# Performance work log

Measured on AMD Instinct MI355X. Metric: run time of the kernel, lower is better.

The kernel has to match this reference:

```python
import jax, jax.numpy as jnp
import numpy as np

B, K, LQ, LR, H = 32, 8, 128, 256, 512  # H = hidden_dim*2
L = LQ + K * LR


def setup_inputs() -> dict:
    key = jax.random.key(0)
    ks = jax.random.split(key, 10)
    w = 0.02
    return {
        "h_q": jax.random.normal(ks[0], (B, LQ, H), jnp.float32),
        "q_mask": jnp.ones((B, LQ), jnp.float32),
        "h_r": jax.random.normal(ks[1], (B, K, LR, H), jnp.float32),
        "r_mask": jnp.ones((B, K, LR), jnp.float32),
        "s_t": jax.random.normal(ks[2], (B, H), jnp.float32),
        "qr_cov": jnp.zeros((B, L), jnp.float32),
        # Linear weights stored torch-style [out, in]
        "U_w": jax.random.normal(ks[3], (H, H), jnp.float32) * w,
        "Wc_w": jax.random.normal(ks[4], (H, 1), jnp.float32) * w,
        "Ws_w": jax.random.normal(ks[5], (H, H), jnp.float32) * w,
        "Wqr_w": jax.random.normal(ks[6], (H, H), jnp.float32) * w,
        "Wqr_b": jax.random.normal(ks[7], (H,), jnp.float32) * w,
        "Vr_w": jax.random.normal(ks[8], (1, H), jnp.float32) * w,
    }


def reference(h_q, q_mask, h_r, r_mask, s_t, qr_cov,
              U_w, Wc_w, Ws_w, Wqr_w, Wqr_b, Vr_w):
    b, l_q, h = h_q.shape
    _, k, l_r, _ = h_r.shape

    _h_q = jnp.broadcast_to(h_q[:, None], (b, k, l_q, h)).reshape(b * k, l_q, h)
    _h_r = h_r.reshape(b * k, l_r, h)
    _q_mask = jnp.broadcast_to(q_mask[:, None], (b, k, l_q)).reshape(b * k, l_q)
    _r_mask = r_mask.reshape(b * k, l_r)

    # bilinear co-attention scores: tanh((hq @ U^T) @ hr^T)  [b*k, l_q, l_r]
    hqU = jnp.einsum('bqi,oi->bqo', _h_q, U_w)
    U = jnp.tanh(jnp.einsum('bqo,bro->bqr', hqU, _h_r))

    alpha_q = jax.nn.softmax(jnp.max(U, axis=2), axis=-1)  # [b*k, l_q]
    alpha_r = jax.nn.softmax(jnp.max(U, axis=1), axis=-1)  # [b*k, l_r]

    pai_q = ((alpha_q * _q_mask)[..., None] * _h_q).reshape(b, k, l_q, h).mean(axis=1)
    pai_r = ((alpha_r * _r_mask)[..., None] * _h_r).reshape(b, k * l_r, h)
    qr = jnp.concatenate([pai_q, pai_r], axis=1)  # [b, L, h]

    dec_fea = (jnp.einsum('bi,oi->bo', s_t, Ws_w)[:, None, :]
               + jnp.einsum('bli,oi->blo', qr, Wqr_w) + Wqr_b
               + qr_cov[:, :, None] * Wc_w[:, 0])  # coverage feature

    logits = jnp.einsum('blo,o->bl', jnp.tanh(dec_fea), Vr_w[0])  # [b, L]
    mask = jnp.concatenate([q_mask, r_mask.reshape(b, k * l_r)], axis=1)
    a = jax.nn.softmax(logits, axis=1) * mask
    a = a / jnp.sum(a, axis=1, keepdims=True)

    c_t = jnp.einsum('bl,blh->bh', a, qr)
    new_cov = qr_cov + a
    return (c_t, a, new_cov)
```

## Files before the change

kernel.cpp:

```cpp
#include <hip/hip_runtime.h>
#include <hip/hip_fp8.h>
#include <stdint.h>

#define B  32
#define KK 8
#define LQ 128
#define LR 256
#define H  512
#define LL 2176

typedef short s16x8 __attribute__((ext_vector_type(8)));
typedef float f32x4 __attribute__((ext_vector_type(4)));
typedef int   i32x8 __attribute__((ext_vector_type(8)));

__device__ __forceinline__ unsigned short f2bf(float f) {
    unsigned int u = __float_as_uint(f);
    unsigned int r = (u + 0x7FFFu + ((u >> 16) & 1u)) >> 16;
    return (unsigned short)r;
}
__device__ __forceinline__ unsigned char f2fp8(float f) {
    __hip_fp8_e4m3 v(f);
    return (unsigned char)v.__x;
}
__device__ __forceinline__ void gload16(const void* g, void* l) {
    __builtin_amdgcn_global_load_lds(
        (const __attribute__((address_space(1))) void*)g,
        (__attribute__((address_space(3))) void*)l, 16, 0, 0);
}
__device__ __forceinline__ float fexp2(float x) {
#if __has_builtin(__builtin_amdgcn_exp2f)
    return __builtin_amdgcn_exp2f(x);
#else
    return __expf(x * 0.69314718056f);
#endif
}
__device__ __forceinline__ float frcp(float x) {
#if __has_builtin(__builtin_amdgcn_rcpf)
    return __builtin_amdgcn_rcpf(x);
#else
    return 1.f / x;
#endif
}
__device__ __forceinline__ float fast_tanh(float x) {
    float e = fexp2(x * 2.885390082f);
    return 1.f - 2.f * frcp(1.f + e);
}
#define LOG2E 1.4426950408889634f

#define NQ4 (B * LQ * H / 4)
#define NR4 (B * KK * LR * H / 4)
#define NW4 (H * H / 4)
#define NL4 (B * LL / 4)
#define NC4 (B * H / 4)
#define NWB4 (B * LL / 4)
#define QBLK 256
#define RBLK 4096
#define WBLK 64
#define ZBLK 19
#define SBLK 256
#define K0GRID (QBLK + RBLK + WBLK + ZBLK + SBLK)
__global__ __launch_bounds__(256) void k0_convert(
    const float* __restrict__ h_q, const float* __restrict__ h_r,
    const float* __restrict__ U_w, const float* __restrict__ Wqr_w,
    unsigned short* __restrict__ Xb, unsigned short* __restrict__ Uwb,
    unsigned short* __restrict__ Wqrb, unsigned char* __restrict__ Xb8,
    unsigned char* __restrict__ Wqrb8, float* __restrict__ logits,
    float* __restrict__ out_ct, float* __restrict__ wbuf,
    const float* __restrict__ s_t, const float* __restrict__ Ws_w,
    float* __restrict__ sWs) {
    int t = threadIdx.x;
    int blk = blockIdx.x;
    ushort4* Xb4 = (ushort4*)Xb;
    uchar4* Xb84 = (uchar4*)Xb8;
    if (blk < QBLK + RBLK) {
        const float4* src; ushort4* dst; uchar4* dst8;
        if (blk < QBLK) {
            unsigned u0 = (unsigned)blk * 2048u;
            unsigned b = (unsigned)blk >> 3;
            unsigned off = b * 278528u + (u0 & 16383u);
            src = (const float4*)h_q + u0;
            dst = Xb4 + off; dst8 = Xb84 + off;
        } else {
            unsigned rb = (unsigned)(blk - QBLK);
            unsigned u0 = rb * 2048u;
            unsigned b = rb >> 7;
            unsigned off = b * 278528u + 16384u + (u0 & 262143u);
            src = (const float4*)h_r + u0;
            dst = Xb4 + off; dst8 = Xb84 + off;
        }
        float4 v[8];
#pragma unroll
        for (int j = 0; j < 8; ++j) v[j] = src[t + j * 256];
#pragma unroll
        for (int j = 0; j < 8; ++j) {
            ushort4 o;
            o.x = f2bf(v[j].x); o.y = f2bf(v[j].y);
            o.z = f2bf(v[j].z); o.w = f2bf(v[j].w);
            dst[t + j * 256] = o;
            uchar4 o8;
            o8.x = f2fp8(v[j].x); o8.y = f2fp8(v[j].y);
            o8.z = f2fp8(v[j].z); o8.w = f2fp8(v[j].w);
            dst8[t + j * 256] = o8;
        }
    } else if (blk < QBLK + RBLK + WBLK) {
        int wb = blk - (QBLK + RBLK);
        bool isU = (wb < 32);
        const float4* src = (isU ? (const float4*)U_w : (const float4*)Wqr_w)
                            + (unsigned)(wb & 31) * 2048u;
        ushort4* dst = (isU ? (ushort4*)Uwb : (ushort4*)Wqrb)
                       + (unsigned)(wb & 31) * 2048u;
        uchar4* dst8 = (uchar4*)Wqrb8 + (unsigned)(wb & 31) * 2048u;
        float4 v[8];
#pragma unroll
        for (int j = 0; j < 8; ++j) v[j] = src[t + j * 256];
#pragma unroll
        for (int j = 0; j < 8; ++j) {
            ushort4 o;
            o.x = f2bf(v[j].x); o.y = f2bf(v[j].y);
            o.z = f2bf(v[j].z); o.w = f2bf(v[j].w);
            dst[t + j * 256] = o;
            if (!isU) {
                uchar4 o8;
                o8.x = f2fp8(v[j].x); o8.y = f2fp8(v[j].y);
                o8.z = f2fp8(v[j].z); o8.w = f2fp8(v[j].w);
                dst8[t + j * 256] = o8;
            }
        }
    } else if (blk < QBLK + RBLK + WBLK + ZBLK) {
        unsigned zb = (unsigned)(blk - (QBLK + RBLK + WBLK));
        float4 zero = {0.f, 0.f, 0.f, 0.f};
        float4* lg4 = (float4*)logits;
        float4* ct4 = (float4*)out_ct;
        float4* wb4 = (float4*)wbuf;
#pragma unroll
        for (int j = 0; j < 8; ++j) {
            unsigned z = zb * 2048u + (unsigned)j * 256u + (unsigned)t;
            if (z < NL4) lg4[z] = zero;
            else if (z < NL4 + NC4) ct4[z - NL4] = zero;
            else if (z < NL4 + NC4 + NWB4) wb4[z - NL4 - NC4] = zero;
        }
    } else {
        int idx = blk - (QBLK + RBLK + WBLK + ZBLK);
        int b = idx >> 3, oc = idx & 7;
        __shared__ __align__(16) float sl[H];
        for (int i = t; i < H; i += 256) sl[i] = s_t[b * H + i];
        __syncthreads();
        int o = oc * 64 + (t >> 2);
        int part = t & 3;
        const float4* sl4 = (const float4*)sl;
        const float4* wr4 = (const float4*)(Ws_w + (size_t)o * H);
        float a = 0.f;
#pragma unroll
        for (int ii = 0; ii < 32; ++ii) {
            int i = part + 4 * ii;
            float4 x = sl4[i], y = wr4[i];
            a += x.x * y.x + x.y * y.y + x.z * y.z + x.w * y.w;
        }
        a += __shfl_xor(a, 1);
        a += __shfl_xor(a, 2);
        if (part == 0) sWs[b * H + o] = a;
    }
}

__global__ __launch_bounds__(256) void k1_gemm_hqU(
    const unsigned short* __restrict__ Xb, const unsigned short* __restrict__ Uwb,
    unsigned short* __restrict__ hqU) {
    __shared__ __align__(16) unsigned short As[64 * 64];
    __shared__ __align__(16) unsigned short Bs[128 * 64];
    int tid = threadIdx.x;
    int wave = tid >> 6, lane = tid & 63;
    int quad = lane >> 4, l16 = lane & 15;
    int wr = wave >> 1, wc = wave & 1;
    int g = blockIdx.x;
    int tle = (g & 7) * 32 + (g >> 3);
    int mt = tle >> 2, nt = tle & 3;
    int m0 = mt * 64, n0 = nt * 128;

    const unsigned short* ag[2]; unsigned short* la[2];
    const unsigned short* bg[4]; unsigned short* lb[4];
#pragma unroll
    for (int i = 0; i < 2; ++i) {
        int gg = (wave * 2 + i) * 64 + lane;
        int r = gg >> 3, c = gg & 7, cs = c ^ (r & 7);
        int am = m0 + r;
        ag[i] = Xb + ((size_t)(am >> 7) * LL + (am & 127)) * H + cs * 8;
        la[i] = As + (wave * 2 + i) * 512;
    }
#pragma unroll
    for (int i = 0; i < 4; ++i) {
        int gg = (wave * 4 + i) * 64 + lane;
        int r = gg >> 3, c = gg & 7, cs = c ^ (r & 7);
        bg[i] = Uwb + (size_t)(n0 + r) * H + cs * 8;
        lb[i] = Bs + (wave * 4 + i) * 512;
    }

    f32x4 acc[2][4] = {};
    for (int k0 = 0; k0 < H; k0 += 64) {
#pragma unroll
        for (int i = 0; i < 2; ++i) gload16(ag[i] + k0, la[i]);
#pragma unroll
        for (int i = 0; i < 4; ++i) gload16(bg[i] + k0, lb[i]);
        __syncthreads();
#pragma unroll
        for (int kh = 0; kh < 2; ++kh) {
            s16x8 af[2], bfr[4];
#pragma unroll
            for (int mi = 0; mi < 2; ++mi) {
                int row = wr * 32 + mi * 16 + l16;
                int ch = (kh * 4 + quad) ^ (row & 7);
                af[mi] = *(const s16x8*)&As[(row * 8 + ch) * 8];
            }
#pragma unroll
            for (int ni = 0; ni < 4; ++ni) {
                int row = wc * 64 + ni * 16 + l16;
                int ch = (kh * 4 + quad) ^ (row & 7);
                bfr[ni] = *(const s16x8*)&Bs[(row * 8 + ch) * 8];
            }
#pragma unroll
            for (int mi = 0; mi < 2; ++mi)
#pragma unroll
                for (int ni = 0; ni < 4; ++ni)
                    acc[mi][ni] = __builtin_amdgcn_mfma_f32_16x16x32_bf16(
                        af[mi], bfr[ni], acc[mi][ni], 0, 0, 0);
        }
        __syncthreads();
    }
#pragma unroll
    for (int mi = 0; mi < 2; ++mi)
#pragma unroll
        for (int ni = 0; ni < 4; ++ni)
#pragma unroll
            for (int i = 0; i < 4; ++i) {
                int row = m0 + wr * 32 + mi * 16 + quad * 4 + i;
                int col = n0 + wc * 64 + ni * 16 + l16;
                hqU[(size_t)row * H + col] = f2bf(acc[mi][ni][i]);
            }
}

__global__ __launch_bounds__(256) void k2_scores(
    const unsigned short* __restrict__ hqU, const unsigned short* __restrict__ Xb,
    float* __restrict__ maxq, float* __restrict__ maxr_part) {
    __shared__ __align__(16) unsigned short As[64 * 64];
    __shared__ __align__(16) unsigned short Bs[256 * 64];
    __shared__ float redA[64 * 2];
    __shared__ float redB[256 * 2];
    int g = blockIdx.x;
    int tle = (g & 7) * 64 + (g >> 3);
    int qt = tle & 1, k = (tle >> 1) & 7, b = tle >> 4;
    int tid = threadIdx.x;
    int wave = tid >> 6, lane = tid & 63;
    int quad = lane >> 4, l16 = lane & 15;
    int wr = wave >> 1, wc = wave & 1;

    const unsigned short* Ab = hqU + (size_t)(b * LQ + qt * 64) * H;
    const unsigned short* Bb = Xb + (size_t)(b * LL + LQ + k * LR) * H;

    const unsigned short* ag[2]; unsigned short* la[2];
    const unsigned short* bg[8]; unsigned short* lb[8];
#pragma unroll
    for (int i = 0; i < 2; ++i) {
        int gg = (wave * 2 + i) * 64 + lane;
        int r = gg >> 3, c = gg & 7, cs = c ^ (r & 7);
        ag[i] = Ab + (size_t)r * H + cs * 8;
        la[i] = As + (wave * 2 + i) * 512;
    }
#pragma unroll
    for (int i = 0; i < 8; ++i) {
        int gg = (wave * 8 + i) * 64 + lane;
        int r = gg >> 3, c = gg & 7, cs = c ^ (r & 7);
        bg[i] = Bb + (size_t)r * H + cs * 8;
        lb[i] = Bs + (wave * 8 + i) * 512;
    }

    f32x4 acc[2][8] = {};
    for (int k0 = 0; k0 < H; k0 += 64) {
#pragma unroll
        for (int i = 0; i < 2; ++i) gload16(ag[i] + k0, la[i]);
#pragma unroll
        for (int i = 0; i < 8; ++i) gload16(bg[i] + k0, lb[i]);
        __syncthreads();
#pragma unroll
        for (int kh = 0; kh < 2; ++kh) {
            s16x8 af[2], bfr[8];
#pragma unroll
            for (int mi = 0; mi < 2; ++mi) {
                int row = wr * 32 + mi * 16 + l16;
                int ch = (kh * 4 + quad) ^ (row & 7);
                af[mi] = *(const s16x8*)&As[(row * 8 + ch) * 8];
            }
#pragma unroll
            for (int ni = 0; ni < 8; ++ni) {
                int row = wc * 128 + ni * 16 + l16;
                int ch = (kh * 4 + quad) ^ (row & 7);
                bfr[ni] = *(const s16x8*)&Bs[(row * 8 + ch) * 8];
            }
#pragma unroll
            for (int mi = 0; mi < 2; ++mi)
#pragma unroll
                for (int ni = 0; ni < 8; ++ni)
                    acc[mi][ni] = __builtin_amdgcn_mfma_f32_16x16x32_bf16(
                        af[mi], bfr[ni], acc[mi][ni], 0, 0, 0);
        }
        __syncthreads();
    }
#pragma unroll
    for (int mi = 0; mi < 2; ++mi)
#pragma unroll
        for (int i = 0; i < 4; ++i) {
            float v = acc[mi][0][i];
#pragma unroll
            for (int ni = 1; ni < 8; ++ni) v = fmaxf(v, acc[mi][ni][i]);
            for (int s = 1; s < 16; s <<= 1) v = fmaxf(v, __shfl_xor(v, s));
            if (l16 == 0) redA[(wr * 32 + mi * 16 + quad * 4 + i) * 2 + wc] = v;
        }
#pragma unroll
    for (int ni = 0; ni < 8; ++ni) {
        float v = acc[0][ni][0];
#pragma unroll
        for (int mi = 0; mi < 2; ++mi)
#pragma unroll
            for (int i = 0; i < 4; ++i) v = fmaxf(v, acc[mi][ni][i]);
        for (int s = 16; s < 64; s <<= 1) v = fmaxf(v, __shfl_xor(v, s));
        if (quad == 0) redB[(wc * 128 + ni * 16 + l16) * 2 + wr] = v;
    }
    __syncthreads();
    size_t bk = (size_t)(b * KK + k);
    if (tid < 64)
        maxq[bk * 128 + qt * 64 + tid] = fmaxf(redA[tid * 2 + 0], redA[tid * 2 + 1]);
    maxr_part[(bk * 2 + qt) * 256 + tid] = fmaxf(redB[tid * 2 + 0], redB[tid * 2 + 1]);
}

__global__ __launch_bounds__(256) void k3_alphas(
    const float* __restrict__ maxq, const float* __restrict__ maxr_part,
    const float* __restrict__ r_mask, const float* __restrict__ q_mask,
    float* __restrict__ wbuf) {
    int b = blockIdx.x >> 3, k = blockIdx.x & 7;
    int t = threadIdx.x;
    __shared__ float red[256];
    size_t bk = (size_t)(b * KK + k);
    float vq = -1e30f;
    if (t < 128) vq = fast_tanh(maxq[bk * 128 + t]);
    red[t] = vq; __syncthreads();
    for (int s = 128; s > 0; s >>= 1) { if (t < s) red[t] = fmaxf(red[t], red[t + s]); __syncthreads(); }
    float mxq = red[0]; __syncthreads();
    float eq = (t < 128) ? fexp2((vq - mxq) * LOG2E) : 0.f;
    red[t] = eq; __syncthreads();
    for (int s = 128; s > 0; s >>= 1) { if (t < s) red[t] += red[t + s]; __syncthreads(); }
    float invq = 1.f / red[0]; __syncthreads();
    if (t < 128)
        atomicAdd(&wbuf[b * LL + t], q_mask[b * LQ + t] * eq * invq * 0.125f);
    float vr = fast_tanh(fmaxf(maxr_part[(bk * 2 + 0) * 256 + t],
                               maxr_part[(bk * 2 + 1) * 256 + t]));
    red[t] = vr; __syncthreads();
    for (int s = 128; s > 0; s >>= 1) { if (t < s) red[t] = fmaxf(red[t], red[t + s]); __syncthreads(); }
    float mxr = red[0]; __syncthreads();
    float er = fexp2((vr - mxr) * LOG2E);
    red[t] = er; __syncthreads();
    for (int s = 128; s > 0; s >>= 1) { if (t < s) red[t] += red[t + s]; __syncthreads(); }
    float invr = 1.f / red[0];
    wbuf[b * LL + LQ + k * LR + t] = r_mask[bk * LR + t] * er * invr;
}

__global__ __launch_bounds__(256) void k4_gemm_logits(
    const unsigned char* __restrict__ Xb8, const unsigned char* __restrict__ Wqrb8,
    const float* __restrict__ sWs, const float* __restrict__ Wqr_b,
    const float* __restrict__ Wc_w, const float* __restrict__ Vr_w,
    const float* __restrict__ wbuf, const float* __restrict__ qr_cov,
    float* __restrict__ logits) {
    __shared__ __align__(16) unsigned char As[128 * 128];
    __shared__ __align__(16) unsigned char Bs[128 * 128];
    __shared__ float wrow[128], covrow[128], sWsl[128], biasl[128], wcl[128], vrl[128];
    int tid = threadIdx.x;
    int wave = tid >> 6, lane = tid & 63;
    int quad = lane >> 4, l16 = lane & 15;
    int wr = wave >> 1, wc = wave & 1;
    int g = blockIdx.x;
    int tle = (g & 7) * 272 + (g >> 3);
    int mt = tle >> 2, nt = tle & 3;
    size_t m0 = (size_t)mt * 128;
    int n0 = nt * 128;
    int b = mt / 17;

    if (tid < 128) {
        wrow[tid]   = wbuf[m0 + tid];
        covrow[tid] = qr_cov[m0 + tid];
        sWsl[tid]   = sWs[b * H + n0 + tid];
        biasl[tid]  = Wqr_b[n0 + tid];
        wcl[tid]    = Wc_w[n0 + tid];
        vrl[tid]    = Vr_w[n0 + tid];
    }

    const unsigned char* ag[4]; unsigned char* la[4];
    const unsigned char* bg[4]; unsigned char* lb[4];
#pragma unroll
    for (int i = 0; i < 4; ++i) {
        int gg = (wave * 4 + i) * 64 + lane;
        int r = gg >> 3, c = gg & 7, cs = c ^ (r & 7);
        ag[i] = Xb8 + (m0 + r) * H + cs * 16;
        bg[i] = Wqrb8 + (size_t)(n0 + r) * H + cs * 16;
        la[i] = As + (wave * 4 + i) * 1024;
        lb[i] = Bs + (wave * 4 + i) * 1024;
    }

    f32x4 acc[4][4] = {};
    for (int k0 = 0; k0 < H; k0 += 128) {
#pragma unroll
        for (int i = 0; i < 4; ++i) gload16(ag[i] + k0, la[i]);
#pragma unroll
        for (int i = 0; i < 4; ++i) gload16(bg[i] + k0, lb[i]);
        __syncthreads();
        i32x8 af[4];
#pragma unroll
        for (int mi = 0; mi < 4; ++mi) {
            int row = wr * 64 + mi * 16 + l16;
            int xs = row & 7;
            const uint4* rp = (const uint4*)(As + row * 128);
            uint4 lo = rp[(quad * 2) ^ xs];
            uint4 hi = rp[(quad * 2 + 1) ^ xs];
            af[mi][0] = lo.x; af[mi][1] = lo.y; af[mi][2] = lo.z; af[mi][3] = lo.w;
            af[mi][4] = hi.x; af[mi][5] = hi.y; af[mi][6] = hi.z; af[mi][7] = hi.w;
        }
#pragma unroll
        for (int ni = 0; ni < 4; ++ni) {
            int row = wc * 64 + ni * 16 + l16;
            int xs = row & 7;
            const uint4* rp = (const uint4*)(Bs + row * 128);
            uint4 lo = rp[(quad * 2) ^ xs];
            uint4 hi = rp[(quad * 2 + 1) ^ xs];
            i32x8 bfr;
            bfr[0] = lo.x; bfr[1] = lo.y; bfr[2] = lo.z; bfr[3] = lo.w;
            bfr[4] = hi.x; bfr[5] = hi.y; bfr[6] = hi.z; bfr[7] = hi.w;
#pragma unroll
            for (int mi = 0; mi < 4; ++mi)
                acc[mi][ni] = __builtin_amdgcn_mfma_scale_f32_16x16x128_f8f6f4(
                    af[mi], bfr, acc[mi][ni], 0, 0,
                    0, 0x7F7F7F7F, 0, 0x7F7F7F7F);
        }
        __syncthreads();
    }
#pragma unroll
    for (int mi = 0; mi < 4; ++mi)
#pragma unroll
        for (int i = 0; i < 4; ++i) {
            int rl = wr * 64 + mi * 16 + quad * 4 + i;
            float wv = wrow[rl], cv = covrow[rl];
            float lsum = 0.f;
#pragma unroll
            for (int ni = 0; ni < 4; ++ni) {
                int ol = wc * 64 + ni * 16 + l16;
                float dec = sWsl[ol] + wv * acc[mi][ni][i] + biasl[ol] + cv * wcl[ol];
                lsum += vrl[ol] * fast_tanh(dec);
            }
            for (int s = 1; s < 16; s <<= 1) lsum += __shfl_xor(lsum, s);
            if (l16 == 0) atomicAdd(&logits[m0 + rl], lsum);
        }
}

__global__ __launch_bounds__(256) void k5a_softmax(
    const float* __restrict__ logits, const float* __restrict__ q_mask,
    const float* __restrict__ r_mask, const float* __restrict__ qr_cov,
    const float* __restrict__ wbuf, float* __restrict__ out,
    float* __restrict__ coef) {
    int b = blockIdx.x, t = threadIdx.x;
    __shared__ float lg[LL];
    __shared__ float red[256];
    float mx = -1e30f;
    for (int l = t; l < LL; l += 256) {
        float v = logits[b * LL + l];
        lg[l] = v;
        mx = fmaxf(mx, v);
    }
    red[t] = mx; __syncthreads();
    for (int s = 128; s > 0; s >>= 1) { if (t < s) red[t] = fmaxf(red[t], red[t + s]); __syncthreads(); }
    mx = red[0]; __syncthreads();
    float sum = 0.f;
    for (int l = t; l < LL; l += 256) {
        float e = fexp2((lg[l] - mx) * LOG2E);
        float m = (l < LQ) ? q_mask[b * LQ + l] : r_mask[b * (KK * LR) + l - LQ];
        float em = e * m;
        lg[l] = em;
        sum += em;
    }
    red[t] = sum; __syncthreads();
    for (int s = 128; s > 0; s >>= 1) { if (t < s) red[t] += red[t + s]; __syncthreads(); }
    float inv = 1.f / red[0];
    __syncthreads();
    float* aout = out + B * H + (size_t)b * LL;
    float* cov  = out + B * H + (size_t)B * LL + (size_t)b * LL;
    for (int l = t; l < LL; l += 256) {
        float a = lg[l] * inv;
        aout[l] = a;
        cov[l] = qr_cov[b * LL + l] + a;
        coef[b * LL + l] = a * wbuf[b * LL + l];
    }
}

__global__ __launch_bounds__(256) void k5b_ct(
    const unsigned short* __restrict__ Xb, const float* __restrict__ coef,
    float* __restrict__ out) {
    int b = blockIdx.x / 34, chunk = blockIdx.x % 34;
    int t = threadIdx.x;
    int l0 = chunk * 64;
    __shared__ float cl[64];
    __shared__ float red[4][512];
    if (t < 64) cl[t] = coef[b * LL + l0 + t];
    __syncthreads();
    int rr = t >> 6, lane = t & 63, cc = lane * 8;
    float a[8] = {};
    const unsigned short* xp = Xb + ((size_t)b * LL + l0) * H;
    for (int l = rr; l < 64; l += 4) {
        float c = cl[l];
        uint4 u4 = *(const uint4*)(xp + (size_t)l * H + cc);
        a[0] += c * __uint_as_float(u4.x << 16);
        a[1] += c * __uint_as_float(u4.x & 0xffff0000u);
        a[2] += c * __uint_as_float(u4.y << 16);
        a[3] += c * __uint_as_float(u4.y & 0xffff0000u);
        a[4] += c * __uint_as_float(u4.z << 16);
        a[5] += c * __uint_as_float(u4.z & 0xffff0000u);
        a[6] += c * __uint_as_float(u4.w << 16);
        a[7] += c * __uint_as_float(u4.w & 0xffff0000u);
    }
#pragma unroll
    for (int j = 0; j < 8; ++j) red[rr][cc + j] = a[j];
    __syncthreads();
    int col = t * 2;
    float s0 = red[0][col] + red[1][col] + red[2][col] + red[3][col];
    float s1 = red[0][col + 1] + red[1][col + 1] + red[2][col + 1] + red[3][col + 1];
    atomicAdd(&out[b * H + col], s0);
    atomicAdd(&out[b * H + col + 1], s1);
}

extern "C" void kernel_launch(void* const* d_in, const int* in_sizes, int n_in,
                              void* d_out, int out_size, void* d_ws, size_t ws_size,
                              hipStream_t stream) {
    (void)in_sizes; (void)n_in; (void)out_size; (void)ws_size;
    const float* h_q    = (const float*)d_in[0];
    const float* q_mask = (const float*)d_in[1];
    const float* h_r    = (const float*)d_in[2];
    const float* r_mask = (const float*)d_in[3];
    const float* s_t    = (const float*)d_in[4];
    const float* qr_cov = (const float*)d_in[5];
    const float* U_w    = (const float*)d_in[6];
    const float* Wc_w   = (const float*)d_in[7];
    const float* Ws_w   = (const float*)d_in[8];
    const float* Wqr_w  = (const float*)d_in[9];
    const float* Wqr_b  = (const float*)d_in[10];
    const float* Vr_w   = (const float*)d_in[11];
    float* out = (float*)d_out;

    char* p = (char*)d_ws;
    unsigned short* Xb    = (unsigned short*)p; p += (size_t)B * LL * H * 2;
    unsigned char*  Xb8   = (unsigned char*)p;  p += (size_t)B * LL * H;
    unsigned short* Uwb   = (unsigned short*)p; p += (size_t)H * H * 2;
    unsigned short* Wqrb  = (unsigned short*)p; p += (size_t)H * H * 2;
    unsigned char*  Wqrb8 = (unsigned char*)p;  p += (size_t)H * H;
    unsigned short* hqU   = (unsigned short*)p; p += (size_t)B * LQ * H * 2;
    float* sWs       = (float*)p; p += (size_t)B * H * 4;
    float* maxq      = (float*)p; p += (size_t)B * KK * 128 * 4;
    float* maxr_part = (float*)p; p += (size_t)B * KK * 2 * 256 * 4;
    float* wbuf      = (float*)p; p += (size_t)B * LL * 4;
    float* logits    = (float*)p; p += (size_t)B * LL * 4;
    float* coef      = (float*)p; p += (size_t)B * LL * 4;

    k0_convert<<<K0GRID, 256, 0, stream>>>(h_q, h_r, U_w, Wqr_w, Xb, Uwb, Wqrb,
                                           Xb8, Wqrb8, logits, out, wbuf,
                                           s_t, Ws_w, sWs);
    k1_gemm_hqU<<<256, 256, 0, stream>>>(Xb, Uwb, hqU);
    k2_scores<<<512, 256, 0, stream>>>(hqU, Xb, maxq, maxr_part);
    k3_alphas<<<B * KK, 256, 0, stream>>>(maxq, maxr_part, r_mask, q_mask, wbuf);
    k4_gemm_logits<<<2176, 256, 0, stream>>>(
        Xb8, Wqrb8, sWs, Wqr_b, Wc_w, Vr_w, wbuf, qr_cov, logits);
    k5a_softmax<<<B, 256, 0, stream>>>(logits, q_mask, r_mask, qr_cov, wbuf, out, coef);
    k5b_ct<<<B * 34, 256, 0, stream>>>(Xb, coef, out);
}
```

Baseline: 360.0 us.

## Switch score GEMM to FP8 MFMA and pack conversions in convert kernel

The bilinear score GEMM now reads hqU and h_r as FP8 e4m3 and uses the 16x16x128 scaled f8f6f4 MFMA with unit scales, which halves operand bytes and K-loop iterations. k1 writes hqU directly as packed FP8. The convert kernel packs bf16/fp8 with wider stores via the packed-convert builtin, drops the unused bf16 Wqr copy, and moves the small blocks ahead of the bulk conversion blocks. The cost is lower precision in the tanh/max scores that drive the attention weights.

Result: no change. 361.2 us (+0.3%).

```diff
diff --git a/kernel.cpp b/kernel.cpp
--- a/kernel.cpp
+++ b/kernel.cpp
@@ -22,6 +22,16 @@
     __hip_fp8_e4m3 v(f);
     return (unsigned char)v.__x;
 }
+__device__ __forceinline__ unsigned int pk_fp8(float a, float b) {
+#if __has_builtin(__builtin_amdgcn_cvt_pk_fp8_f32)
+    return (unsigned int)__builtin_amdgcn_cvt_pk_fp8_f32(a, b, 0, false) & 0xFFFFu;
+#else
+    return (unsigned int)f2fp8(a) | ((unsigned int)f2fp8(b) << 8);
+#endif
+}
+__device__ __forceinline__ unsigned int pk_bf16(float a, float b) {
+    return (unsigned int)f2bf(a) | ((unsigned int)f2bf(b) << 16);
+}
 __device__ __forceinline__ void gload16(const void* g, void* l) {
     __builtin_amdgcn_global_load_lds(
         (const __attribute__((address_space(1))) void*)g,
@@ -49,85 +59,75 @@
 
 #define NQ4 (B * LQ * H / 4)
 #define NR4 (B * KK * LR * H / 4)
-#define NW4 (H * H / 4)
 #define NL4 (B * LL / 4)
 #define NC4 (B * H / 4)
 #define NWB4 (B * LL / 4)
+#define SBLK 256
+#define WBLK 64
+#define ZBLK 19
 #define QBLK 256
 #define RBLK 4096
-#define WBLK 64
-#define ZBLK 19
-#define SBLK 256
-#define K0GRID (QBLK + RBLK + WBLK + ZBLK + SBLK)
+#define K0GRID (SBLK + WBLK + ZBLK + QBLK + RBLK)
 __global__ __launch_bounds__(256) void k0_convert(
     const float* __restrict__ h_q, const float* __restrict__ h_r,
     const float* __restrict__ U_w, const float* __restrict__ Wqr_w,
     unsigned short* __restrict__ Xb, unsigned short* __restrict__ Uwb,
-    unsigned short* __restrict__ Wqrb, unsigned char* __restrict__ Xb8,
-    unsigned char* __restrict__ Wqrb8, float* __restrict__ logits,
-    float* __restrict__ out_ct, float* __restrict__ wbuf,
-    const float* __restrict__ s_t, const float* __restrict__ Ws_w,
-    float* __restrict__ sWs) {
+    unsigned char* __restrict__ Xb8, unsigned char* __restrict__ Wqrb8,
+    float* __restrict__ logits, float* __restrict__ out_ct,
+    float* __restrict__ wbuf, const float* __restrict__ s_t,
+    const float* __restrict__ Ws_w, float* __restrict__ sWs) {
     int t = threadIdx.x;
     int blk = blockIdx.x;
-    ushort4* Xb4 = (ushort4*)Xb;
-    uchar4* Xb84 = (uchar4*)Xb8;
-    if (blk < QBLK + RBLK) {
-        const float4* src; ushort4* dst; uchar4* dst8;
-        if (blk < QBLK) {
-            unsigned u0 = (unsigned)blk * 2048u;
-            unsigned b = (unsigned)blk >> 3;
-            unsigned off = b * 278528u + (u0 & 16383u);
-            src = (const float4*)h_q + u0;
-            dst = Xb4 + off; dst8 = Xb84 + off;
-        } else {
-            unsigned rb = (unsigned)(blk - QBLK);
-            unsigned u0 = rb * 2048u;
-            unsigned b = rb >> 7;
-            unsigned off = b * 278528u + 16384u + (u0 & 262143u);
-            src = (const float4*)h_r + u0;
-            dst = Xb4 + off; dst8 = Xb84 + off;
-        }
-        float4 v[8];
-#pragma unroll
-        for (int j = 0; j < 8; ++j) v[j] = src[t + j * 256];
-#pragma unroll
-        for (int j = 0; j < 8; ++j) {
-            ushort4 o;
-            o.x = f2bf(v[j].x); o.y = f2bf(v[j].y);
-            o.z = f2bf(v[j].z); o.w = f2bf(v[j].w);
-            dst[t + j * 256] = o;
-            uchar4 o8;
-            o8.x = f2fp8(v[j].x); o8.y = f2fp8(v[j].y);
-            o8.z = f2fp8(v[j].z); o8.w = f2fp8(v[j].w);
-            dst8[t + j * 256] = o8;
-        }
-    } else if (blk < QBLK + RBLK + WBLK) {
-        int wb = blk - (QBLK + RBLK);
-        bool isU = (wb < 32);
-        const float4* src = (isU ? (const float4*)U_w : (const float4*)Wqr_w)
-                            + (unsigned)(wb & 31) * 2048u;
-        ushort4* dst = (isU ? (ushort4*)Uwb : (ushort4*)Wqrb)
-                       + (unsigned)(wb & 31) * 2048u;
-        uchar4* dst8 = (uchar4*)Wqrb8 + (unsigned)(wb & 31) * 2048u;
-        float4 v[8];
-#pragma unroll
-        for (int j = 0; j < 8; ++j) v[j] = src[t + j * 256];
-#pragma unroll
-        for (int j = 0; j < 8; ++j) {
-            ushort4 o;
-            o.x = f2bf(v[j].x); o.y = f2bf(v[j].y);
-            o.z = f2bf(v[j].z); o.w = f2bf(v[j].w);
-            dst[t + j * 256] = o;
-            if (!isU) {
-                uchar4 o8;
-                o8.x = f2fp8(v[j].x); o8.y = f2fp8(v[j].y);
-                o8.z = f2fp8(v[j].z); o8.w = f2fp8(v[j].w);
-                dst8[t + j * 256] = o8;
+    if (blk < SBLK) {
+        int b = blk >> 3, oc = blk & 7;
+        __shared__ __align__(16) float sl[H];
+        for (int i = t; i < H; i += 256) sl[i] = s_t[b * H + i];
+        __syncthreads();
+        int o = oc * 64 + (t >> 2);
+        int part = t & 3;
+        const float4* sl4 = (const float4*)sl;
+        const float4* wr4 = (const float4*)(Ws_w + (size_t)o * H);
+        float a = 0.f;
+#pragma unroll
+        for (int ii = 0; ii < 32; ++ii) {
+            int i = part + 4 * ii;
+            float4 x = sl4[i], y = wr4[i];
+            a += x.x * y.x + x.y * y.y + x.z * y.z + x.w * y.w;
+        }
+        a += __shfl_xor(a, 1);
+        a += __shfl_xor(a, 2);
+        if (part == 0) sWs[b * H + o] = a;
+        return;
+    }
+    blk -= SBLK;
+    if (blk < WBLK) {
+        bool isU = (blk < 32);
+        unsigned base = (unsigned)(blk & 31) * 2048u;
+        const float4* src = isU ? (const float4*)U_w : (const float4*)Wqr_w;
+        uint4* dst = isU ? (uint4*)Uwb : (uint4*)((unsigned short*)Xb + 0);
+        uint4* dstW = (uint4*)((unsigned char*)0);
+        (void)dstW;
+#pragma unroll
+        for (int jj = 0; jj < 4; ++jj) {
+            unsigned f4i = base + (unsigned)jj * 512u + 2u * (unsigned)t;
+            float4 v0 = src[f4i], v1 = src[f4i + 1];
+            uint4 ob;
+            ob.x = pk_bf16(v0.x, v0.y); ob.y = pk_bf16(v0.z, v0.w);
+            ob.z = pk_bf16(v1.x, v1.y); ob.w = pk_bf16(v1.z, v1.w);
+            if (isU) {
+                ((uint4*)Uwb)[f4i >> 1] = ob;
+            } else {
+                uint2 o8;
+                o8.x = pk_fp8(v0.x, v0.y) | (pk_fp8(v0.z, v0.w) << 16);
+                o8.y = pk_fp8(v1.x, v1.y) | (pk_fp8(v1.z, v1.w) << 16);
+                ((uint2*)Wqrb8)[f4i >> 1] = o8;
             }
         }
-    } else if (blk < QBLK + RBLK + WBLK + ZBLK) {
-        unsigned zb = (unsigned)(blk - (QBLK + RBLK + WBLK));
+        return;
+    }
+    blk -= WBLK;
+    if (blk < ZBLK) {
+        unsigned zb = (unsigned)blk;
         float4 zero = {0.f, 0.f, 0.f, 0.f};
         float4* lg4 = (float4*)logits;
         float4* ct4 = (float4*)out_ct;
@@ -139,32 +139,45 @@
             else if (z < NL4 + NC4) ct4[z - NL4] = zero;
             else if (z < NL4 + NC4 + NWB4) wb4[z - NL4 - NC4] = zero;
         }
-    } else {
-        int idx = blk - (QBLK + RBLK + WBLK + ZBLK);
-        int b = idx >> 3, oc = idx & 7;
-        __shared__ __align__(16) float sl[H];
-        for (int i = t; i < H; i += 256) sl[i] = s_t[b * H + i];
-        __syncthreads();
-        int o = oc * 64 + (t >> 2);
-        int part = t & 3;
-        const float4* sl4 = (const float4*)sl;
-        const float4* wr4 = (const float4*)(Ws_w + (size_t)o * H);
-        float a = 0.f;
-#pragma unroll
-        for (int ii = 0; ii < 32; ++ii) {
-            int i = part + 4 * ii;
-            float4 x = sl4[i], y = wr4[i];
-            a += x.x * y.x + x.y * y.y + x.z * y.z + x.w * y.w;
-        }
-        a += __shfl_xor(a, 1);
-        a += __shfl_xor(a, 2);
-        if (part == 0) sWs[b * H + o] = a;
+        return;
+    }
+    blk -= ZBLK;
+    {
+        const float4* src; unsigned dstoff;
+        if (blk < QBLK) {
+            unsigned u0 = (unsigned)blk * 2048u;
+            unsigned b = (unsigned)blk >> 3;
+            src = (const float4*)h_q + u0;
+            dstoff = b * 278528u + (u0 & 16383u);
+        } else {
+            unsigned rb = (unsigned)(blk - QBLK);
+            unsigned u0 = rb * 2048u;
+            unsigned b = rb >> 7;
+            src = (const float4*)h_r + u0;
+            dstoff = b * 278528u + 16384u + (u0 & 262143u);
+        }
+        uint4* dstb = (uint4*)Xb;
+        uint2* dst8 = (uint2*)Xb8;
+#pragma unroll
+        for (int jj = 0; jj < 4; ++jj) {
+            unsigned loc = (unsigned)jj * 512u + 2u * (unsigned)t;
+            float4 v0 = src[loc], v1 = src[loc + 1];
+            unsigned idx = (dstoff + loc) >> 1;
+            uint4 ob;
+            ob.x = pk_bf16(v0.x, v0.y); ob.y = pk_bf16(v0.z, v0.w);
+            ob.z = pk_bf16(v1.x, v1.y); ob.w = pk_bf16(v1.z, v1.w);
+            dstb[idx] = ob;
+            uint2 o8;
+            o8.x = pk_fp8(v0.x, v0.y) | (pk_fp8(v0.z, v0.w) << 16);
+            o8.y = pk_fp8(v1.x, v1.y) | (pk_fp8(v1.z, v1.w) << 16);
+            dst8[idx] = o8;
+        }
     }
 }
 
 __global__ __launch_bounds__(256) void k1_gemm_hqU(
     const unsigned short* __restrict__ Xb, const unsigned short* __restrict__ Uwb,
-    unsigned short* __restrict__ hqU) {
+    unsigned char* __restrict__ hqU8) {
     __shared__ __align__(16) unsigned short As[64 * 64];
     __shared__ __align__(16) unsigned short Bs[128 * 64];
     int tid = threadIdx.x;
@@ -231,17 +244,22 @@
         for (int ni = 0; ni < 4; ++ni)
 #pragma unroll
             for (int i = 0; i < 4; ++i) {
-                int row = m0 + wr * 32 + mi * 16 + quad * 4 + i;
-                int col = n0 + wc * 64 + ni * 16 + l16;
-                hqU[(size_t)row * H + col] = f2bf(acc[mi][ni][i]);
+                float v = acc[mi][ni][i];
+                float vn = __shfl_xor(v, 1);
+                if ((l16 & 1) == 0) {
+                    int row = m0 + wr * 32 + mi * 16 + quad * 4 + i;
+                    int col = n0 + wc * 64 + ni * 16 + l16;
+                    unsigned short pk = (unsigned short)pk_fp8(v, vn);
+                    *(unsigned short*)(hqU8 + (size_t)row * H + col) = pk;
+                }
             }
 }
 
 __global__ __launch_bounds__(256) void k2_scores(
-    const unsigned short* __restrict__ hqU, const unsigned short* __restrict__ Xb,
+    const unsigned char* __restrict__ hqU8, const unsigned char* __restrict__ Xb8,
     float* __restrict__ maxq, float* __restrict__ maxr_part) {
-    __shared__ __align__(16) unsigned short As[64 * 64];
-    __shared__ __align__(16) unsigned short Bs[256 * 64];
+    __shared__ __align__(16) unsigned char As[64 * 128];
+    __shared__ __align__(16) unsigned char Bs[256 * 128];
     __shared__ float redA[64 * 2];
     __shared__ float redB[256 * 2];
     int g = blockIdx.x;
@@ -252,54 +270,59 @@
     int quad = lane >> 4, l16 = lane & 15;
     int wr = wave >> 1, wc = wave & 1;
 
-    const unsigned short* Ab = hqU + (size_t)(b * LQ + qt * 64) * H;
-    const unsigned short* Bb = Xb + (size_t)(b * LL + LQ + k * LR) * H;
-
-    const unsigned short* ag[2]; unsigned short* la[2];
-    const unsigned short* bg[8]; unsigned short* lb[8];
+    const unsigned char* Ab = hqU8 + (size_t)(b * LQ + qt * 64) * H;
+    const unsigned char* Bb = Xb8 + (size_t)(b * LL + LQ + k * LR) * H;
+
+    const unsigned char* ag[2]; unsigned char* la[2];
+    const unsigned char* bg[8]; unsigned char* lb[8];
 #pragma unroll
     for (int i = 0; i < 2; ++i) {
         int gg = (wave * 2 + i) * 64 + lane;
         int r = gg >> 3, c = gg & 7, cs = c ^ (r & 7);
-        ag[i] = Ab + (size_t)r * H + cs * 8;
-        la[i] = As + (wave * 2 + i) * 512;
+        ag[i] = Ab + (size_t)r * H + cs * 16;
+        la[i] = As + gg * 16;
     }
 #pragma unroll
     for (int i = 0; i < 8; ++i) {
         int gg = (wave * 8 + i) * 64 + lane;
         int r = gg >> 3, c = gg & 7, cs = c ^ (r & 7);
-        bg[i] = Bb + (size_t)r * H + cs * 8;
-        lb[i] = Bs + (wave * 8 + i) * 512;
+        bg[i] = Bb + (size_t)r * H + cs * 16;
+        lb[i] = Bs + gg * 16;
     }
 
     f32x4 acc[2][8] = {};
-    for (int k0 = 0; k0 < H; k0 += 64) {
+    for (int k0 = 0; k0 < H; k0 += 128) {
 #pragma unroll
         for (int i = 0; i < 2; ++i) gload16(ag[i] + k0, la[i]);
 #pragma unroll
         for (int i = 0; i < 8; ++i) gload16(bg[i] + k0, lb[i]);
         __syncthreads();
-#pragma unroll
-        for (int kh = 0; kh < 2; ++kh) {
-            s16x8 af[2], bfr[8];
-#pragma unroll
-            for (int mi = 0; mi < 2; ++mi) {
-                int row = wr * 32 + mi * 16 + l16;
-                int ch = (kh * 4 + quad) ^ (row & 7);
-                af[mi] = *(const s16x8*)&As[(row * 8 + ch) * 8];
-            }
-#pragma unroll
-            for (int ni = 0; ni < 8; ++ni) {
-                int row = wc * 128 + ni * 16 + l16;
-                int ch = (kh * 4 + quad) ^ (row & 7);
-                bfr[ni] = *(const s16x8*)&Bs[(row * 8 + ch) * 8];
-            }
+        i32x8 af[2];
+#pragma unroll
+        for (int mi = 0; mi < 2; ++mi) {
+            int row = wr * 32 + mi * 16 + l16;
+            int xs = row & 7;
+            const uint4* rp = (const uint4*)(As + row * 128);
+            uint4 lo = rp[(quad * 2) ^ xs];
+            uint4 hi = rp[(quad * 2 + 1) ^ xs];
+            af[mi][0] = lo.x; af[mi][1] = lo.y; af[mi][2] = lo.z; af[mi][3] = lo.w;
+            af[mi][4] = hi.x; af[mi][5] = hi.y; af[mi][6] = hi.z; af[mi][7] = hi.w;
+        }
+#pragma unroll
+        for (int ni = 0; ni < 8; ++ni) {
+            int row = wc * 128 + ni * 16 + l16;
+            int xs = row & 7;
+            const uint4* rp = (const uint4*)(Bs + row * 128);
+            uint4 lo = rp[(quad * 2) ^ xs];
+            uint4 hi = rp[(quad * 2 + 1) ^ xs];
+            i32x8 bfr;
+            bfr[0] = lo.x; bfr[1] = lo.y; bfr[2] = lo.z; bfr[3] = lo.w;
+            bfr[4] = hi.x; bfr[5] = hi.y; bfr[6] = hi.z; bfr[7] = hi.w;
 #pragma unroll
             for (int mi = 0; mi < 2; ++mi)
-#pragma unroll
-                for (int ni = 0; ni < 8; ++ni)
-                    acc[mi][ni] = __builtin_amdgcn_mfma_f32_16x16x32_bf16(
-                        af[mi], bfr[ni], acc[mi][ni], 0, 0, 0);
+                acc[mi][ni] = __builtin_amdgcn_mfma_scale_f32_16x16x128_f8f6f4(
+                    af[mi], bfr, acc[mi][ni], 0, 0,
+                    0, 0x7F7F7F7F, 0, 0x7F7F7F7F);
         }
         __syncthreads();
     }
@@ -552,9 +575,8 @@
     unsigned short* Xb    = (unsigned short*)p; p += (size_t)B * LL * H * 2;
     unsigned char*  Xb8   = (unsigned char*)p;  p += (size_t)B * LL * H;
     unsigned short* Uwb   = (unsigned short*)p; p += (size_t)H * H * 2;
-    unsigned short* Wqrb  = (unsigned short*)p; p += (size_t)H * H * 2;
     unsigned char*  Wqrb8 = (unsigned char*)p;  p += (size_t)H * H;
-    unsigned short* hqU   = (unsigned short*)p; p += (size_t)B * LQ * H * 2;
+    unsigned char*  hqU8  = (unsigned char*)p;  p += (size_t)B * LQ * H;
     float* sWs       = (float*)p; p += (size_t)B * H * 4;
     float* maxq      = (float*)p; p += (size_t)B * KK * 128 * 4;
     float* maxr_part = (float*)p; p += (size_t)B * KK * 2 * 256 * 4;
@@ -562,11 +584,11 @@
     float* logits    = (float*)p; p += (size_t)B * LL * 4;
     float* coef      = (float*)p; p += (size_t)B * LL * 4;
 
-    k0_convert<<<K0GRID, 256, 0, stream>>>(h_q, h_r, U_w, Wqr_w, Xb, Uwb, Wqrb,
+    k0_convert<<<K0GRID, 256, 0, stream>>>(h_q, h_r, U_w, Wqr_w, Xb, Uwb,
                                            Xb8, Wqrb8, logits, out, wbuf,
                                            s_t, Ws_w, sWs);
-    k1_gemm_hqU<<<256, 256, 0, stream>>>(Xb, Uwb, hqU);
-    k2_scores<<<512, 256, 0, stream>>>(hqU, Xb, maxq, maxr_part);
+    k1_gemm_hqU<<<256, 256, 0, stream>>>(Xb, Uwb, hqU8);
+    k2_scores<<<512, 256, 0, stream>>>(hqU8, Xb8, maxq, maxr_part);
     k3_alphas<<<B * KK, 256, 0, stream>>>(maxq, maxr_part, r_mask, q_mask, wbuf);
     k4_gemm_logits<<<2176, 256, 0, stream>>>(
         Xb8, Wqrb8, sWs, Wqr_b, Wc_w, Vr_w, wbuf, qr_cov, logits);
```
